# Kernel optimization log

Measured on AMD Instinct MI355X. Metric: run time of the kernel, lower is better.

Reference implementation:

```python
import jax, jax.numpy as jnp
import numpy as np

B, S, DIN, D, H, L, DFF = 256, 100, 64, 256, 8, 6, 1024
DK = D // H
SCALE = float(np.sqrt(DK))

def _pe(s, d):
    pos = np.arange(s)[:, None].astype(np.float32)
    div = np.exp(np.arange(0, d, 2).astype(np.float32) * (-np.log(10000.0) / d))
    pe = np.zeros((s, d), np.float32)
    pe[:, 0::2] = np.sin(pos * div)
    pe[:, 1::2] = np.cos(pos * div)
    return jnp.asarray(pe)

PE = _pe(S, D)  # (S, D) sinusoidal positional encoding

def _ln(x, g, b, eps=1e-5):
    m = jnp.mean(x, -1, keepdims=True)
    v = jnp.mean((x - m) ** 2, -1, keepdims=True)
    return (x - m) * jax.lax.rsqrt(v + eps) * g + b

def setup_inputs() -> dict:
    ks = iter(jax.random.split(jax.random.key(0), 32))
    def w(*shape):
        return jax.random.normal(next(ks), shape, jnp.float32) * 0.02
    z = lambda *s: jnp.zeros(s, jnp.float32)
    o = lambda *s: jnp.ones(s, jnp.float32)
    return {
        'x': jax.random.normal(next(ks), (B, S, DIN), jnp.float32),
        'W_in': w(DIN, D), 'b_in': z(D),
        'Wq': w(L, D, D), 'bq': z(L, D),
        'Wk': w(L, D, D), 'bk': z(L, D),
        'Wv': w(L, D, D), 'bv': z(L, D),
        'Wo': w(L, D, D), 'bo': z(L, D),
        'g1': o(L, D), 'be1': z(L, D),
        'W1': w(L, D, DFF), 'b1': z(L, DFF),
        'W2': w(L, DFF, D), 'b2': z(L, D),
        'g2': o(L, D), 'be2': z(L, D),
        'lnf_g': o(D), 'lnf_b': z(D),
        'Wr1': w(D, 128), 'br1': z(128), 'Wr2': w(128, 3), 'br2': z(3),
        'Wa1': w(D, 128), 'ba1': z(128), 'Wa2': w(128, 64), 'ba2': z(64), 'Wa3': w(64, 1), 'ba3': z(1),
        'Wc1': w(D, 64), 'bc1': z(64), 'Wc2': w(64, 1), 'bc2': z(1),
        'Wv1': w(D, 64), 'bv1': z(64), 'Wv2': w(64, 1), 'bv2': z(1),
    }

def reference(x, W_in, b_in, Wq, bq, Wk, bk, Wv, bv, Wo, bo, g1, be1, W1, b1, W2, b2, g2, be2, lnf_g, lnf_b, Wr1, br1, Wr2, br2, Wa1, ba1, Wa2, ba2, Wa3, ba3, Wc1, bc1, Wc2, bc2, Wv1, bv1, Wv2, bv2):
    h = x @ W_in + b_in + PE  # (B, S, D); dropout is identity in eval mode

    def block(h, p):
        wq, bq_, wk, bk_, wv, bv_, wo, bo_, g1_, be1_, w1, b1_, w2, b2_, g2_, be2_ = p
        q = (h @ wq + bq_).reshape(B, S, H, DK)
        k = (h @ wk + bk_).reshape(B, S, H, DK)
        v = (h @ wv + bv_).reshape(B, S, H, DK)
        s = jnp.einsum('bqhd,bkhd->bhqk', q, k) / SCALE
        a = jax.nn.softmax(s, axis=-1)
        o = jnp.einsum('bhqk,bkhd->bqhd', a, v).reshape(B, S, D)
        h = _ln(h + o @ wo + bo_, g1_, be1_)
        f = jax.nn.relu(h @ w1 + b1_) @ w2 + b2_
        h = _ln(h + f, g2_, be2_)
        return h, None

    h, _ = jax.lax.scan(block, h, (Wq, bq, Wk, bk, Wv, bv, Wo, bo, g1, be1, W1, b1, W2, b2, g2, be2))
    h = _ln(h, lnf_g, lnf_b)
    hf = h[:, -1]  # seq_lengths=None -> last token
    regime = jax.nn.softmax(jax.nn.relu(hf @ Wr1 + br1) @ Wr2 + br2, axis=-1)
    action = jnp.tanh(jax.nn.relu(jax.nn.relu(hf @ Wa1 + ba1) @ Wa2 + ba2) @ Wa3 + ba3)
    confidence = jax.nn.sigmoid(jax.nn.relu(hf @ Wc1 + bc1) @ Wc2 + bc2)
    volatility = jax.nn.relu(jax.nn.relu(hf @ Wv1 + bv1) @ Wv2 + bv2)
    return action, regime, confidence, volatility, hf
```

## Files before the change

### kernel.cpp

```cpp
#include <hip/hip_runtime.h>
#include <hip/hip_bf16.h>

#define BB   256
#define SS   100
#define DIN  64
#define DD   256
#define HH   8
#define LL   6
#define DFF  1024
#define MM   (BB*SS)
#define INV_SCALE 0.17677669529663687f

typedef unsigned short u16;
typedef __attribute__((__ext_vector_type__(8))) __bf16 bf16x8;
typedef __attribute__((__ext_vector_type__(8))) unsigned short u16x8;
typedef __attribute__((__ext_vector_type__(4))) float  f32x4;

__device__ __forceinline__ u16 f2bf(float f) {
    unsigned u = __float_as_uint(f);
    u += 0x7FFFu + ((u >> 16) & 1u);
    return (u16)(u >> 16);
}
__device__ __forceinline__ float bf2f(u16 v) {
    return __uint_as_float((unsigned)v << 16);
}

#define MFMA16(a,b,c) __builtin_amdgcn_mfma_f32_16x16x32_bf16((a),(b),(c),0,0,0)

#if defined(__has_builtin)
#if __has_builtin(__builtin_amdgcn_global_load_lds)
#define HAVE_GLDS 1
#endif
#endif

#ifdef HAVE_GLDS
typedef __attribute__((address_space(1))) const void gas_void;
typedef __attribute__((address_space(3))) void las_void;
__device__ __forceinline__ void gload16(const u16* g, u16* l) {
    __builtin_amdgcn_global_load_lds((gas_void*)g, (las_void*)l, 16, 0, 0);
}
#else
__device__ __forceinline__ void gload16(const u16* g, u16* l) {
    const int lane = threadIdx.x & 63;
    *(uint4*)((char*)l + lane * 16) = *(const uint4*)g;
}
#endif

__global__ void pe_init_kernel(float* __restrict__ pe) {
    int i = blockIdx.x * blockDim.x + threadIdx.x;
    if (i >= SS * DD) return;
    int s = i >> 8;
    int c = i & 255;
    int ce = c & ~1;
    double div = exp((double)ce * -0.03597789207803197);
    double ang = (double)s * div;
    pe[i] = (float)((c & 1) ? cos(ang) : sin(ang));
}

__global__ void conv_bf16(const float* __restrict__ in, u16* __restrict__ out, int n) {
    int i = blockIdx.x * 256 + threadIdx.x;
    if (i < n) out[i] = f2bf(in[i]);
}

__global__ __launch_bounds__(256)
void transpose_conv(const float* __restrict__ in, u16* __restrict__ out,
                    int K, int N, long outLstride) {
    __shared__ float tile[32][33];
    const int k0 = blockIdx.x * 32, n0 = blockIdx.y * 32, lz = blockIdx.z;
    const int tx = threadIdx.x & 31, ty = threadIdx.x >> 5;
    const float* src = in + (size_t)lz * K * N;
#pragma unroll
    for (int i = 0; i < 4; ++i)
        tile[ty + i*8][tx] = src[(size_t)(k0 + ty + i*8) * N + n0 + tx];
    __syncthreads();
    u16* dst = out + (size_t)lz * outLstride;
#pragma unroll
    for (int i = 0; i < 4; ++i)
        dst[(size_t)(n0 + ty + i*8) * K + k0 + tx] = f2bf(tile[tx][ty + i*8]);
}

__global__ void pack_bias(const float* __restrict__ bq, const float* __restrict__ bk,
                          const float* __restrict__ bv, float* __restrict__ bqkv) {
    int idx = blockIdx.x * 256 + threadIdx.x;
    if (idx >= LL * 768) return;
    int l = idx / 768, c = idx % 768;
    float v = (c < 256) ? bq[l*256 + c] : (c < 512) ? bk[l*256 + c - 256] : bv[l*256 + c - 512];
    bqkv[idx] = v;
}

__global__ void pack_wh1(const float* __restrict__ Wr1, const float* __restrict__ Wa1,
                         const float* __restrict__ Wc1, const float* __restrict__ Wv1,
                         const float* __restrict__ br1, const float* __restrict__ ba1,
                         const float* __restrict__ bc1, const float* __restrict__ bv1,
                         u16* __restrict__ Wh1T, float* __restrict__ bh1) {
    int i = blockIdx.x * 256 + threadIdx.x;
    if (i < 384 * 256) {
        int n = i >> 8, k = i & 255;
        float v = (n < 128) ? Wr1[k*128 + n]
                : (n < 256) ? Wa1[k*128 + (n-128)]
                : (n < 320) ? Wc1[k*64  + (n-256)]
                            : Wv1[k*64  + (n-320)];
        Wh1T[(size_t)n * 256 + k] = f2bf(v);
    }
    if (i < 384) {
        float v = (i < 128) ? br1[i] : (i < 256) ? ba1[i-128]
                : (i < 320) ? bc1[i-256] : bv1[i-320];
        bh1[i] = v;
    }
}

template<int EPI, bool OF32, bool OBF16>
__global__ __launch_bounds__(256)
void mfma_gemm(const u16* __restrict__ A, const u16* __restrict__ Wt,
               const float* __restrict__ bias, const float* __restrict__ pe,
               float* __restrict__ Cf, u16* __restrict__ Cb,
               int M, int N, int K) {
    __shared__ u16 As[2][128 * 32];
    __shared__ u16 Bs[2][128 * 32];
    const int t = threadIdx.x, w = t >> 6, l = t & 63;
    const int bm = blockIdx.x * 128, bn = blockIdx.y * 128;
    const int wr = (w >> 1) * 64, wc = (w & 1) * 64;
    const int lr = l & 15, lk = (l >> 4) * 8, lq = (l >> 4) * 4;
    const int srow = l >> 2, scol = (l & 3) * 8;

    f32x4 acc[4][4] = {};
    const u16* Ag = &A [(size_t)(bm + w * 32 + srow) * K + scol];
    const u16* Bg = &Wt[(size_t)(bn + w * 32 + srow) * K + scol];

    auto stage = [&](int buf, int k0) {
        gload16(Ag + k0,                  &As[buf][(w * 32) * 32]);
        gload16(Ag + k0 + (size_t)16 * K, &As[buf][(w * 32 + 16) * 32]);
        gload16(Bg + k0,                  &Bs[buf][(w * 32) * 32]);
        gload16(Bg + k0 + (size_t)16 * K, &Bs[buf][(w * 32 + 16) * 32]);
    };

    stage(0, 0);
    if (32 < K) stage(1, 32);
    int cur = 0;

    for (int k0 = 0; k0 < K; k0 += 32) {
        if (k0 + 32 < K) asm volatile("s_waitcnt vmcnt(4)" ::: "memory");
        else             asm volatile("s_waitcnt vmcnt(0)" ::: "memory");
        __builtin_amdgcn_s_barrier();

        bf16x8 af[4], bfr[4];
#pragma unroll
        for (int m = 0; m < 4; ++m) af[m]  = *(const bf16x8*)&As[cur][(wr + m*16 + lr) * 32 + lk];
#pragma unroll
        for (int n = 0; n < 4; ++n) bfr[n] = *(const bf16x8*)&Bs[cur][(wc + n*16 + lr) * 32 + lk];
#pragma unroll
        for (int m = 0; m < 4; ++m)
#pragma unroll
            for (int n = 0; n < 4; ++n)
                acc[m][n] = MFMA16(af[m], bfr[n], acc[m][n]);

        __builtin_amdgcn_s_barrier();
        if (k0 + 64 < K) stage(cur, k0 + 64);
        cur ^= 1;
    }

#pragma unroll
    for (int n = 0; n < 4; ++n) {
        const int col = bn + wc + n*16 + lr;
        const float bv = bias[col];
#pragma unroll
        for (int m = 0; m < 4; ++m) {
#pragma unroll
            for (int j = 0; j < 4; ++j) {
                const int row = bm + wr + m*16 + lq + j;
                float v = acc[m][n][j] + bv;
                if (EPI == 1) v = fmaxf(v, 0.f);
                if (EPI == 2) v += pe[(row % SS) * DD + col];
                if (OF32)  Cf[(size_t)row * N + col] = v;
                if (OBF16) Cb[(size_t)row * N + col] = f2bf(v);
            }
        }
    }
}

__global__ __launch_bounds__(512)
void gemm_ln(const u16* __restrict__ A, const u16* __restrict__ Wt,
             const float* __restrict__ bias, const float* __restrict__ g,
             const float* __restrict__ be, u16* __restrict__ hb, int K) {
    __shared__ u16 As[2][64 * 32];
    __shared__ u16 Bs[2][256 * 32];
    __shared__ float red[64][8];
    const int t = threadIdx.x, w = t >> 6, l = t & 63;
    const int bm = blockIdx.x * 64;
    const int wr = w >> 2, wc = w & 3;
    const int lr = l & 15, lk = (l >> 4) * 8, lq = (l >> 4) * 4;
    const int crow = l >> 2, ccol = (l & 3) * 8;

    const int c0 = (w < 4) ? 3*w : 12 + 2*(w - 4);
    const int nc = (w < 4) ? 3 : 2;

    f32x4 acc[2][4] = {};

    auto stage = [&](int buf, int k0) {
        for (int ci = 0; ci < nc; ++ci) {
            const int c = c0 + ci;
            if (c < 4)
                gload16(&A [(size_t)(bm + c*16 + crow) * K + k0 + ccol], &As[buf][c*16*32]);
            else
                gload16(&Wt[(size_t)((c-4)*16 + crow) * K + k0 + ccol], &Bs[buf][(c-4)*16*32]);
        }
    };

    stage(0, 0);
    if (32 < K) stage(1, 32);
    int cur = 0;

    for (int k0 = 0; k0 < K; k0 += 32) {
        if (k0 + 32 < K) {
            if (w < 4) asm volatile("s_waitcnt vmcnt(3)" ::: "memory");
            else       asm volatile("s_waitcnt vmcnt(2)" ::: "memory");
        } else {
            asm volatile("s_waitcnt vmcnt(0)" ::: "memory");
        }
        __builtin_amdgcn_s_barrier();

        bf16x8 af[2], bf[4];
#pragma unroll
        for (int mf = 0; mf < 2; ++mf) af[mf] = *(const bf16x8*)&As[cur][(wr*32 + mf*16 + lr) * 32 + lk];
#pragma unroll
        for (int n = 0; n < 4; ++n)    bf[n]  = *(const bf16x8*)&Bs[cur][(wc*64 + n*16 + lr) * 32 + lk];
#pragma unroll
        for (int mf = 0; mf < 2; ++mf)
#pragma unroll
            for (int n = 0; n < 4; ++n)
                acc[mf][n] = MFMA16(af[mf], bf[n], acc[mf][n]);

        __builtin_amdgcn_s_barrier();
        if (k0 + 64 < K) stage(cur, k0 + 64);
        cur ^= 1;
    }

    float bv[4], gv[4], bev[4];
#pragma unroll
    for (int n = 0; n < 4; ++n) {
        int col = wc*64 + n*16 + lr;
        bv[n] = bias[col]; gv[n] = g[col]; bev[n] = be[col];
    }
#pragma unroll
    for (int mf = 0; mf < 2; ++mf) {
#pragma unroll
        for (int j = 0; j < 4; ++j) {
            const int rloc = wr*32 + mf*16 + lq + j;
            const int row  = bm + rloc;
            float s1 = 0.f, s2 = 0.f;
#pragma unroll
            for (int n = 0; n < 4; ++n) {
                float v = acc[mf][n][j] + bv[n] + bf2f(hb[(size_t)row * DD + wc*64 + n*16 + lr]);
                acc[mf][n][j] = v;
                s1 += v; s2 += v * v;
            }
            s1 += __shfl_xor(s1, 1); s2 += __shfl_xor(s2, 1);
            s1 += __shfl_xor(s1, 2); s2 += __shfl_xor(s2, 2);
            s1 += __shfl_xor(s1, 4); s2 += __shfl_xor(s2, 4);
            s1 += __shfl_xor(s1, 8); s2 += __shfl_xor(s2, 8);
            if (lr == 0) { red[rloc][wc*2] = s1; red[rloc][wc*2+1] = s2; }
        }
    }
    __syncthreads();
#pragma unroll
    for (int mf = 0; mf < 2; ++mf) {
#pragma unroll
        for (int j = 0; j < 4; ++j) {
            const int rloc = wr*32 + mf*16 + lq + j;
            const int row  = bm + rloc;
            float s1 = red[rloc][0] + red[rloc][2] + red[rloc][4] + red[rloc][6];
            float s2 = red[rloc][1] + red[rloc][3] + red[rloc][5] + red[rloc][7];
            float mean = s1 * (1.f/DD);
            float var  = s2 * (1.f/DD) - mean*mean;
            float rstd = rsqrtf(var + 1e-5f);
#pragma unroll
            for (int n = 0; n < 4; ++n) {
                int col = wc*64 + n*16 + lr;
                float y = (acc[mf][n][j] - mean) * rstd * gv[n] + bev[n];
                hb[(size_t)row * DD + col] = f2bf(y);
            }
        }
    }
}

__global__ __launch_bounds__(256)
void attn_mfma(const u16* __restrict__ qkv, u16* __restrict__ ao) {
    const int b = blockIdx.x >> 3, hh = blockIdx.x & 7;
    const int t = threadIdx.x, w = t >> 6, l = t & 63;
    const int lr = l & 15, lk = (l >> 4) * 8, lq = (l >> 4) * 4;
    __shared__ u16 Vt[32 * 136];
    __shared__ u16 Ps[4][32 * 136];
    const size_t rbase = (size_t)b * SS * 768;
    const int qc = hh * 32, kc = 256 + hh * 32, vc = 512 + hh * 32;

    for (int u = t; u < 400; u += 256) {
        int s = u >> 2, dp = (u & 3) * 8;
        u16x8 vv = *(const u16x8*)&qkv[rbase + (size_t)s * 768 + vc + dp];
#pragma unroll
        for (int e = 0; e < 8; ++e) Vt[(dp + e) * 136 + s] = vv[e];
    }
    for (int i = t; i < 32 * 36; i += 256) {
        int d = i / 36, s2 = 100 + i % 36;
        Vt[d * 136 + s2] = 0;
    }

    u16x8 qz = {0,0,0,0,0,0,0,0};
    u16x8 qfr[2];
#pragma unroll
    for (int m = 0; m < 2; ++m) {
        int r = w * 32 + m * 16 + lr;
        qfr[m] = (r < SS) ? *(const u16x8*)&qkv[rbase + (size_t)r * 768 + qc + lk] : qz;
    }

    f32x4 sacc[2][7] = {};
#pragma unroll
    for (int n = 0; n < 7; ++n) {
        int r = n * 16 + lr;
        u16x8 kfr = (r < SS) ? *(const u16x8*)&qkv[rbase + (size_t)r * 768 + kc + lk] : qz;
#pragma unroll
        for (int m = 0; m < 2; ++m)
            sacc[m][n] = MFMA16(*(bf16x8*)&qfr[m], *(bf16x8*)&kfr, sacc[m][n]);
    }

#pragma unroll
    for (int m = 0; m < 2; ++m) {
#pragma unroll
        for (int j = 0; j < 4; ++j) {
            float mx = -1e30f;
#pragma unroll
            for (int n = 0; n < 7; ++n) {
                float s = sacc[m][n][j] * INV_SCALE;
                if (n == 6 && lr >= 4) s = -1e30f;
                sacc[m][n][j] = s;
                mx = fmaxf(mx, s);
            }
            mx = fmaxf(mx, __shfl_xor(mx, 1));
            mx = fmaxf(mx, __shfl_xor(mx, 2));
            mx = fmaxf(mx, __shfl_xor(mx, 4));
            mx = fmaxf(mx, __shfl_xor(mx, 8));
            float sum = 0.f;
#pragma unroll
            for (int n = 0; n < 7; ++n) {
                float p = expf(sacc[m][n][j] - mx);
                if (n == 6 && lr >= 4) p = 0.f;
                sacc[m][n][j] = p;
                sum += p;
            }
            sum += __shfl_xor(sum, 1);
            sum += __shfl_xor(sum, 2);
            sum += __shfl_xor(sum, 4);
            sum += __shfl_xor(sum, 8);
            float inv = 1.f / sum;
#pragma unroll
            for (int n = 0; n < 7; ++n) sacc[m][n][j] *= inv;
        }
    }

    u16* myP = &Ps[w][0];
    for (int i = l; i < 32 * 24; i += 64) {
        int r = i / 24, c2 = 112 + i % 24;
        myP[r * 136 + c2] = 0;
    }
#pragma unroll
    for (int m = 0; m < 2; ++m)
#pragma unroll
        for (int n = 0; n < 7; ++n)
#pragma unroll
            for (int j = 0; j < 4; ++j)
                myP[(m*16 + lq + j) * 136 + n*16 + lr] = f2bf(sacc[m][n][j]);

    __syncthreads();

    f32x4 oacc[2][2] = {};
#pragma unroll
    for (int ks = 0; ks < 4; ++ks) {
        bf16x8 pf[2], vf[2];
#pragma unroll
        for (int m = 0; m < 2; ++m) pf[m] = *(const bf16x8*)&myP[(m*16 + lr) * 136 + ks*32 + lk];
#pragma unroll
        for (int n = 0; n < 2; ++n) vf[n] = *(const bf16x8*)&Vt [(n*16 + lr) * 136 + ks*32 + lk];
#pragma unroll
        for (int m = 0; m < 2; ++m)
#pragma unroll
            for (int n = 0; n < 2; ++n)
                oacc[m][n] = MFMA16(pf[m], vf[n], oacc[m][n]);
    }
#pragma unroll
    for (int m = 0; m < 2; ++m)
#pragma unroll
        for (int j = 0; j < 4; ++j) {
            int s = w*32 + m*16 + lq + j;
            if (s < SS) {
#pragma unroll
                for (int n = 0; n < 2; ++n)
                    ao[((size_t)(b*SS + s)) * DD + hh*32 + n*16 + lr] = f2bf(oacc[m][n][j]);
            }
        }
}

__global__ __launch_bounds__(256)
void lastrow_ln(const u16* __restrict__ hb, const float* __restrict__ g,
                const float* __restrict__ be, float* __restrict__ out,
                u16* __restrict__ hfb) {
    const int b = blockIdx.x;
    const int c = threadIdx.x;
    float x = bf2f(hb[(size_t)(b * SS + SS - 1) * DD + c]);

    float s1 = x, s2 = x * x;
#pragma unroll
    for (int o = 32; o > 0; o >>= 1) {
        s1 += __shfl_down(s1, o);
        s2 += __shfl_down(s2, o);
    }
    __shared__ float w1[4], w2[4];
    __shared__ float mean_s, rstd_s;
    const int wid = c >> 6, lane = c & 63;
    if (lane == 0) { w1[wid] = s1; w2[wid] = s2; }
    __syncthreads();
    if (c == 0) {
        float t1 = w1[0] + w1[1] + w1[2] + w1[3];
        float t2 = w2[0] + w2[1] + w2[2] + w2[3];
        float m = t1 * (1.0f / DD);
        float v = t2 * (1.0f / DD) - m * m;
        mean_s = m;
        rstd_s = rsqrtf(v + 1e-5f);
    }
    __syncthreads();
    float y = (x - mean_s) * rstd_s * g[c] + be[c];
    out[1536 + b * DD + c] = y;
    hfb[b * DD + c] = f2bf(y);
}

__global__ __launch_bounds__(256)
void heads2_kernel(const float* __restrict__ t1f,
                   const float* __restrict__ Wr2, const float* __restrict__ br2,
                   const float* __restrict__ Wa2, const float* __restrict__ ba2,
                   const float* __restrict__ Wa3, const float* __restrict__ ba3,
                   const float* __restrict__ Wc2, const float* __restrict__ bc2,
                   const float* __restrict__ Wv2, const float* __restrict__ bv2,
                   float* __restrict__ out) {
    const int b = blockIdx.x, t = threadIdx.x;
    __shared__ float t1[384];
    __shared__ float a2[64];
    __shared__ float lg[3];
    for (int i = t; i < 384; i += 256) t1[i] = t1f[(size_t)b * 384 + i];
    __syncthreads();

    if (t < 64) {
        float acc = ba2[t];
        for (int k = 0; k < 128; ++k) acc = fmaf(t1[128 + k], Wa2[k * 64 + t], acc);
        a2[t] = fmaxf(acc, 0.f);
    } else if (t == 64) {
        float acc = bc2[0];
        for (int k = 0; k < 64; ++k) acc = fmaf(t1[256 + k], Wc2[k], acc);
        out[1024 + b] = 1.0f / (1.0f + expf(-acc));
    } else if (t == 65) {
        float acc = bv2[0];
        for (int k = 0; k < 64; ++k) acc = fmaf(t1[320 + k], Wv2[k], acc);
        out[1280 + b] = fmaxf(acc, 0.f);
    } else if (t >= 66 && t < 69) {
        int r = t - 66;
        float acc = br2[r];
        for (int k = 0; k < 128; ++k) acc = fmaf(t1[k], Wr2[k * 3 + r], acc);
        lg[r] = acc;
    }
    __syncthreads();
    if (t == 0) {
        float m = fmaxf(lg[0], fmaxf(lg[1], lg[2]));
        float e0 = expf(lg[0] - m), e1 = expf(lg[1] - m), e2 = expf(lg[2] - m);
        float inv = 1.0f / (e0 + e1 + e2);
        out[256 + b * 3 + 0] = e0 * inv;
        out[256 + b * 3 + 1] = e1 * inv;
        out[256 + b * 3 + 2] = e2 * inv;
    }
    if (t < 64) {
        float p = a2[t] * Wa3[t];
        p += __shfl_xor(p, 1);
        p += __shfl_xor(p, 2);
        p += __shfl_xor(p, 4);
        p += __shfl_xor(p, 8);
        p += __shfl_xor(p, 16);
        p += __shfl_xor(p, 32);
        if (t == 0) out[b] = tanhf(p + ba3[0]);
    }
}

extern "C" void kernel_launch(void* const* d_in, const int* in_sizes, int n_in,
                              void* d_out, int out_size, void* d_ws, size_t ws_size,
                              hipStream_t stream) {
    const float* x    = (const float*)d_in[0];
    const float* W_in = (const float*)d_in[1];
    const float* b_in = (const float*)d_in[2];
    const float* Wq   = (const float*)d_in[3];
    const float* bq   = (const float*)d_in[4];
    const float* Wk   = (const float*)d_in[5];
    const float* bk   = (const float*)d_in[6];
    const float* Wv   = (const float*)d_in[7];
    const float* bv   = (const float*)d_in[8];
    const float* Wo   = (const float*)d_in[9];
    const float* bo   = (const float*)d_in[10];
    const float* g1   = (const float*)d_in[11];
    const float* be1  = (const float*)d_in[12];
    const float* W1   = (const float*)d_in[13];
    const float* b1   = (const float*)d_in[14];
    const float* W2   = (const float*)d_in[15];
    const float* b2   = (const float*)d_in[16];
    const float* g2   = (const float*)d_in[17];
    const float* be2  = (const float*)d_in[18];
    const float* lnf_g = (const float*)d_in[19];
    const float* lnf_b = (const float*)d_in[20];
    const float* Wr1  = (const float*)d_in[21];
    const float* br1  = (const float*)d_in[22];
    const float* Wr2  = (const float*)d_in[23];
    const float* br2  = (const float*)d_in[24];
    const float* Wa1  = (const float*)d_in[25];
    const float* ba1  = (const float*)d_in[26];
    const float* Wa2  = (const float*)d_in[27];
    const float* ba2  = (const float*)d_in[28];
    const float* Wa3  = (const float*)d_in[29];
    const float* ba3  = (const float*)d_in[30];
    const float* Wc1  = (const float*)d_in[31];
    const float* bc1  = (const float*)d_in[32];
    const float* Wc2  = (const float*)d_in[33];
    const float* bc2  = (const float*)d_in[34];
    const float* Wv1  = (const float*)d_in[35];
    const float* bv1  = (const float*)d_in[36];
    const float* Wv2  = (const float*)d_in[37];
    const float* bv2  = (const float*)d_in[38];
    float* out = (float*)d_out;

    char* w8 = (char*)d_ws;
    float* pe    = (float*)w8;  w8 += (size_t)SS * DD * 4;
    u16*   hb    = (u16*)w8;    w8 += (size_t)MM * DD * 2;
    u16*   xb    = (u16*)w8;    w8 += (size_t)MM * DIN * 2;
    u16*   qkvb  = (u16*)w8;    w8 += (size_t)MM * 768 * 2;
    u16*   ao    = (u16*)w8;    w8 += (size_t)MM * DD * 2;
    u16*   ffn1b = (u16*)w8;    w8 += (size_t)MM * DFF * 2;
    u16*   WinT  = (u16*)w8;    w8 += (size_t)DIN * DD * 2;
    u16*   WqkvT = (u16*)w8;    w8 += (size_t)LL * 768 * DD * 2;
    u16*   WoT   = (u16*)w8;    w8 += (size_t)LL * DD * DD * 2;
    u16*   W1T   = (u16*)w8;    w8 += (size_t)LL * DFF * DD * 2;
    u16*   W2T   = (u16*)w8;    w8 += (size_t)LL * DD * DFF * 2;
    float* bqkv  = (float*)w8;  w8 += (size_t)LL * 768 * 4;
    u16*   Wh1T  = (u16*)w8;    w8 += (size_t)384 * 256 * 2;
    float* bh1   = (float*)w8;  w8 += (size_t)384 * 4;
    u16*   hfb   = (u16*)w8;    w8 += (size_t)BB * DD * 2;
    float* t1f   = (float*)w8;  w8 += (size_t)BB * 384 * 4;

    pe_init_kernel<<<(SS * DD + 255) / 256, 256, 0, stream>>>(pe);
    conv_bf16<<<(MM * DIN + 255) / 256, 256, 0, stream>>>(x, xb, MM * DIN);
    transpose_conv<<<dim3(DIN/32, DD/32, 1), 256, 0, stream>>>(W_in, WinT, DIN, DD, (long)DIN * DD);
    transpose_conv<<<dim3(8, 8, 6),  256, 0, stream>>>(Wq, WqkvT,             DD, DD, 768L * DD);
    transpose_conv<<<dim3(8, 8, 6),  256, 0, stream>>>(Wk, WqkvT + DD*DD,     DD, DD, 768L * DD);
    transpose_conv<<<dim3(8, 8, 6),  256, 0, stream>>>(Wv, WqkvT + 2*DD*DD,   DD, DD, 768L * DD);
    transpose_conv<<<dim3(8, 8, 6),  256, 0, stream>>>(Wo, WoT, DD, DD, (long)DD * DD);
    transpose_conv<<<dim3(8, 32, 6), 256, 0, stream>>>(W1, W1T, DD, DFF, (long)DD * DFF);
    transpose_conv<<<dim3(32, 8, 6), 256, 0, stream>>>(W2, W2T, DFF, DD, (long)DD * DFF);
    pack_bias<<<(LL * 768 + 255) / 256, 256, 0, stream>>>(bq, bk, bv, bqkv);
    pack_wh1<<<384, 256, 0, stream>>>(Wr1, Wa1, Wc1, Wv1, br1, ba1, bc1, bv1, Wh1T, bh1);

    mfma_gemm<2, false, true><<<dim3(MM/128, DD/128), 256, 0, stream>>>(
        xb, WinT, b_in, pe, nullptr, hb, MM, DD, DIN);

    for (int l = 0; l < LL; ++l) {
        mfma_gemm<0, false, true><<<dim3(MM/128, 768/128), 256, 0, stream>>>(
            hb, WqkvT + (size_t)l*768*DD, bqkv + l*768, nullptr, nullptr, qkvb, MM, 768, DD);
        attn_mfma<<<BB * HH, 256, 0, stream>>>(qkvb, ao);
        gemm_ln<<<MM/64, 512, 0, stream>>>(
            ao, WoT + (size_t)l*DD*DD, bo + l*DD, g1 + l*DD, be1 + l*DD, hb, DD);
        mfma_gemm<1, false, true><<<dim3(MM/128, DFF/128), 256, 0, stream>>>(
            hb, W1T + (size_t)l*DFF*DD, b1 + l*DFF, nullptr, nullptr, ffn1b, MM, DFF, DD);
        gemm_ln<<<MM/64, 512, 0, stream>>>(
            ffn1b, W2T + (size_t)l*DD*DFF, b2 + l*DD, g2 + l*DD, be2 + l*DD, hb, DFF);
    }

    lastrow_ln<<<BB, 256, 0, stream>>>(hb, lnf_g, lnf_b, out, hfb);

    mfma_gemm<1, true, false><<<dim3(2, 3), 256, 0, stream>>>(
        hfb, Wh1T, bh1, nullptr, t1f, nullptr, 256, 384, 256);

    heads2_kernel<<<BB, 256, 0, stream>>>(t1f,
        Wr2, br2, Wa2, ba2, Wa3, ba3, Wc2, bc2, Wv2, bv2, out);
}
```

Baseline: 882.0 us.

## Triple-buffer GEMM LDS staging and XOR-swizzle shared-memory layout

Both the generic MFMA GEMM and the fused GEMM+LayerNorm kernel move from double to triple buffering of the A/B tiles. Loads are issued two stages ahead and the vmcnt waits are adjusted to match. The LDS layout is also XOR-swizzled on the 8-element column chunk, consistently on store and load, to cut bank conflicts on the fragment reads. In exchange LDS use per block grows by half, which may reduce occupancy.

```diff
diff --git a/kernel.cpp b/kernel.cpp
--- a/kernel.cpp
+++ b/kernel.cpp
@@ -115,13 +115,14 @@
                const float* __restrict__ bias, const float* __restrict__ pe,
                float* __restrict__ Cf, u16* __restrict__ Cb,
                int M, int N, int K) {
-    __shared__ u16 As[2][128 * 32];
-    __shared__ u16 Bs[2][128 * 32];
+    __shared__ u16 As[3][128 * 32];
+    __shared__ u16 Bs[3][128 * 32];
     const int t = threadIdx.x, w = t >> 6, l = t & 63;
     const int bm = blockIdx.x * 128, bn = blockIdx.y * 128;
     const int wr = (w >> 1) * 64, wc = (w & 1) * 64;
-    const int lr = l & 15, lk = (l >> 4) * 8, lq = (l >> 4) * 4;
-    const int srow = l >> 2, scol = (l & 3) * 8;
+    const int lr = l & 15, lq = (l >> 4) * 4;
+    const int lks = (((l >> 4) ^ ((lr >> 1) & 3)) * 8);
+    const int srow = l >> 2, scol = (((l & 3) ^ ((l >> 3) & 3)) * 8);
 
     f32x4 acc[4][4] = {};
     const u16* Ag = &A [(size_t)(bm + w * 32 + srow) * K + scol];
@@ -135,19 +136,22 @@
     };
 
     stage(0, 0);
-    if (32 < K) stage(1, 32);
+    if (K > 32) stage(1, 32);
+    if (K > 64) stage(2, 64);
     int cur = 0;
 
     for (int k0 = 0; k0 < K; k0 += 32) {
-        if (k0 + 32 < K) asm volatile("s_waitcnt vmcnt(4)" ::: "memory");
-        else             asm volatile("s_waitcnt vmcnt(0)" ::: "memory");
+        const int rem = (K - k0) >> 5;
+        if (rem > 2)       asm volatile("s_waitcnt vmcnt(8)" ::: "memory");
+        else if (rem == 2) asm volatile("s_waitcnt vmcnt(4)" ::: "memory");
+        else               asm volatile("s_waitcnt vmcnt(0)" ::: "memory");
         __builtin_amdgcn_s_barrier();
 
         bf16x8 af[4], bfr[4];
 #pragma unroll
-        for (int m = 0; m < 4; ++m) af[m]  = *(const bf16x8*)&As[cur][(wr + m*16 + lr) * 32 + lk];
-#pragma unroll
-        for (int n = 0; n < 4; ++n) bfr[n] = *(const bf16x8*)&Bs[cur][(wc + n*16 + lr) * 32 + lk];
+        for (int m = 0; m < 4; ++m) af[m]  = *(const bf16x8*)&As[cur][(wr + m*16 + lr) * 32 + lks];
+#pragma unroll
+        for (int n = 0; n < 4; ++n) bfr[n] = *(const bf16x8*)&Bs[cur][(wc + n*16 + lr) * 32 + lks];
 #pragma unroll
         for (int m = 0; m < 4; ++m)
 #pragma unroll
@@ -155,8 +159,8 @@
                 acc[m][n] = MFMA16(af[m], bfr[n], acc[m][n]);
 
         __builtin_amdgcn_s_barrier();
-        if (k0 + 64 < K) stage(cur, k0 + 64);
-        cur ^= 1;
+        if (k0 + 96 < K) stage(cur, k0 + 96);
+        cur = (cur == 2) ? 0 : cur + 1;
     }
 
 #pragma unroll
@@ -182,14 +186,15 @@
 void gemm_ln(const u16* __restrict__ A, const u16* __restrict__ Wt,
              const float* __restrict__ bias, const float* __restrict__ g,
              const float* __restrict__ be, u16* __restrict__ hb, int K) {
-    __shared__ u16 As[2][64 * 32];
-    __shared__ u16 Bs[2][256 * 32];
+    __shared__ u16 As[3][64 * 32];
+    __shared__ u16 Bs[3][256 * 32];
     __shared__ float red[64][8];
     const int t = threadIdx.x, w = t >> 6, l = t & 63;
     const int bm = blockIdx.x * 64;
     const int wr = w >> 2, wc = w & 3;
-    const int lr = l & 15, lk = (l >> 4) * 8, lq = (l >> 4) * 4;
-    const int crow = l >> 2, ccol = (l & 3) * 8;
+    const int lr = l & 15, lq = (l >> 4) * 4;
+    const int lks = (((l >> 4) ^ ((lr >> 1) & 3)) * 8);
+    const int crow = l >> 2, ccol = (((l & 3) ^ ((l >> 3) & 3)) * 8);
 
     const int c0 = (w < 4) ? 3*w : 12 + 2*(w - 4);
     const int nc = (w < 4) ? 3 : 2;
@@ -207,11 +212,16 @@
     };
 
     stage(0, 0);
-    if (32 < K) stage(1, 32);
+    if (K > 32) stage(1, 32);
+    if (K > 64) stage(2, 64);
     int cur = 0;
 
     for (int k0 = 0; k0 < K; k0 += 32) {
-        if (k0 + 32 < K) {
+        const int rem = (K - k0) >> 5;
+        if (rem > 2) {
+            if (w < 4) asm volatile("s_waitcnt vmcnt(6)" ::: "memory");
+            else       asm volatile("s_waitcnt vmcnt(4)" ::: "memory");
+        } else if (rem == 2) {
             if (w < 4) asm volatile("s_waitcnt vmcnt(3)" ::: "memory");
             else       asm volatile("s_waitcnt vmcnt(2)" ::: "memory");
         } else {
@@ -221,9 +231,9 @@
 
         bf16x8 af[2], bf[4];
 #pragma unroll
-        for (int mf = 0; mf < 2; ++mf) af[mf] = *(const bf16x8*)&As[cur][(wr*32 + mf*16 + lr) * 32 + lk];
-#pragma unroll
-        for (int n = 0; n < 4; ++n)    bf[n]  = *(const bf16x8*)&Bs[cur][(wc*64 + n*16 + lr) * 32 + lk];
+        for (int mf = 0; mf < 2; ++mf) af[mf] = *(const bf16x8*)&As[cur][(wr*32 + mf*16 + lr) * 32 + lks];
+#pragma unroll
+        for (int n = 0; n < 4; ++n)    bf[n]  = *(const bf16x8*)&Bs[cur][(wc*64 + n*16 + lr) * 32 + lks];
 #pragma unroll
         for (int mf = 0; mf < 2; ++mf)
 #pragma unroll
@@ -231,8 +241,8 @@
                 acc[mf][n] = MFMA16(af[mf], bf[n], acc[mf][n]);
 
         __builtin_amdgcn_s_barrier();
-        if (k0 + 64 < K) stage(cur, k0 + 64);
-        cur ^= 1;
+        if (k0 + 96 < K) stage(cur, k0 + 96);
+        cur = (cur == 2) ? 0 : cur + 1;
     }
 
     float bv[4], gv[4], bev[4];
```

Measured after the change: 866.0 us. No clear change (-1.8%).
